# Performance work log

Hardware: AMD Instinct MI355X
Metric: run time of the kernel (lower is better)

Reference implementation:

```python
import jax, jax.numpy as jnp
import numpy as np

N, K, D, H = 65536, 8, 128, 128  # nodes, children per node, input_dim, hidden_dim


def setup_inputs() -> dict:
    key = jax.random.key(0)
    ks = jax.random.split(key, 16)
    s = 1.0 / np.sqrt(H)
    inp = {
        "x": jax.random.normal(ks[0], (N, D), jnp.float32),
        "child_h": jax.random.normal(ks[1], (N, K, H), jnp.float32),
        "child_c": jax.random.normal(ks[2], (N, K, H), jnp.float32),
        "Wi": jax.random.normal(ks[3], (D, H), jnp.float32) * s,
        "bi": jax.random.normal(ks[4], (H,), jnp.float32) * s,
        "Ui": jax.random.normal(ks[5], (H, H), jnp.float32) * s,
        "Wo": jax.random.normal(ks[6], (D, H), jnp.float32) * s,
        "bo": jax.random.normal(ks[7], (H,), jnp.float32) * s,
        "Uo": jax.random.normal(ks[8], (H, H), jnp.float32) * s,
        "Wu": jax.random.normal(ks[9], (D, H), jnp.float32) * s,
        "bu": jax.random.normal(ks[10], (H,), jnp.float32) * s,
        "Uu": jax.random.normal(ks[11], (H, H), jnp.float32) * s,
        "Wf": jax.random.normal(ks[12], (D, H), jnp.float32) * s,
        "bf": jax.random.normal(ks[13], (H,), jnp.float32) * s,
        "Uf": jax.random.normal(ks[14], (H, H), jnp.float32) * s,
    }
    return inp


def reference(x, child_h, child_c, Wi, bi, Ui, Wo, bo, Uo, Wu, bu, Uu, Wf, bf, Uf):
    # Child-sum TreeLSTM, batched over N nodes with K children each.
    h_sum = child_h.sum(axis=1)                                  # [N, H]
    i = jax.nn.sigmoid(x @ Wi + bi + h_sum @ Ui)                 # [N, H]
    o = jax.nn.sigmoid(x @ Wo + bo + h_sum @ Uo)                 # [N, H]
    u = jnp.tanh(x @ Wu + bu + h_sum @ Uu)                       # [N, H]
    # Per-child forget gates: f_k = sigmoid(W_f x + U_f h_k)
    f = jax.nn.sigmoid((x @ Wf + bf)[:, None, :]
                       + jnp.einsum("nkh,hd->nkd", child_h, Uf))  # [N, K, H]
    c = i * u + jnp.sum(f * child_c, axis=1)                     # [N, H]
    h = o * jnp.tanh(c)
    return h, c
```

## Files before the change

### kernel.cpp

```cpp
#include <hip/hip_runtime.h>


typedef __attribute__((ext_vector_type(8))) __bf16 bf16x8;
typedef __attribute__((ext_vector_type(4))) float f32x4;

namespace {
constexpr int kK = 8;
constexpr int kD = 128;
constexpr int kH = 128;
constexpr int kM = 16;
constexpr int kBlk = 512;

constexpr int CH_HI = 0;
constexpr int CH_LO = 32768;
constexpr int HS_HI = 65536;
constexpr int HS_LO = 69632;
constexpr int XS_HI = 73728;
constexpr int XS_LO = 77824;
constexpr int GSTRIDE = 132;
constexpr int G_IU = 81920;
constexpr int G_O  = G_IU + 16 * GSTRIDE * 4;
constexpr int G_FX = G_O  + 16 * GSTRIDE * 4;
constexpr int SMEM_SZ = G_FX + 16 * GSTRIDE * 4;
}

__device__ __forceinline__ unsigned f2bf(float f) {
  unsigned u = __float_as_uint(f);
  return (u + 0x7fffu + ((u >> 16) & 1u)) >> 16;
}
__device__ __forceinline__ float bf2f(unsigned h) {
  return __uint_as_float(h << 16);
}
__device__ __forceinline__ float sig_(float z) {
  return 1.0f / (1.0f + __expf(-z));
}
__device__ __forceinline__ float th_(float z) {
  return 1.0f - 2.0f / (__expf(2.0f * z) + 1.0f);
}
__device__ __forceinline__ f32x4 mfma16(bf16x8 a, bf16x8 b, f32x4 c) {
  return __builtin_amdgcn_mfma_f32_16x16x32_bf16(a, b, c, 0, 0, 0);
}

__device__ __forceinline__ int swzOff(int row, int kByte) {
  return row * 256 + (kByte ^ ((row & 15) << 4));
}

__device__ __forceinline__ void split8(const float4& a, const float4& b,
                                       uint4& hi, uint4& lo) {
  const unsigned h0 = f2bf(a.x), h1 = f2bf(a.y), h2 = f2bf(a.z), h3 = f2bf(a.w);
  const unsigned h4 = f2bf(b.x), h5 = f2bf(b.y), h6 = f2bf(b.z), h7 = f2bf(b.w);
  hi = make_uint4(h0 | (h1 << 16), h2 | (h3 << 16), h4 | (h5 << 16),
                  h6 | (h7 << 16));
  const unsigned l0 = f2bf(a.x - bf2f(h0)), l1 = f2bf(a.y - bf2f(h1));
  const unsigned l2 = f2bf(a.z - bf2f(h2)), l3 = f2bf(a.w - bf2f(h3));
  const unsigned l4 = f2bf(b.x - bf2f(h4)), l5 = f2bf(b.y - bf2f(h5));
  const unsigned l6 = f2bf(b.z - bf2f(h6)), l7 = f2bf(b.w - bf2f(h7));
  lo = make_uint4(l0 | (l1 << 16), l2 | (l3 << 16), l4 | (l5 << 16),
                  l6 | (l7 << 16));
}

__device__ __forceinline__ void store_split4(const float4& v, void* hp,
                                             void* lp) {
  const unsigned h0 = f2bf(v.x), h1 = f2bf(v.y), h2 = f2bf(v.z), h3 = f2bf(v.w);
  *reinterpret_cast<uint2*>(hp) = make_uint2(h0 | (h1 << 16), h2 | (h3 << 16));
  const unsigned l0 = f2bf(v.x - bf2f(h0)), l1 = f2bf(v.y - bf2f(h1));
  const unsigned l2 = f2bf(v.z - bf2f(h2)), l3 = f2bf(v.w - bf2f(h3));
  *reinterpret_cast<uint2*>(lp) = make_uint2(l0 | (l1 << 16), l2 | (l3 << 16));
}

__device__ __forceinline__ bf16x8 ldfrag(const unsigned char* base, int row,
                                         int kB) {
  return __builtin_bit_cast(
      bf16x8, *reinterpret_cast<const uint4*>(base + swzOff(row, kB)));
}

__global__ __launch_bounds__(256) void pack_weights(
    const float* __restrict__ Wi, const float* __restrict__ Wo,
    const float* __restrict__ Wu, const float* __restrict__ Wf,
    const float* __restrict__ Ui, const float* __restrict__ Uo,
    const float* __restrict__ Uu, const float* __restrict__ Uf,
    uint4* __restrict__ out) {
  const int gid = blockIdx.x * 256 + threadIdx.x;
  const int lane = gid & 63;
  const int fid = gid >> 6;
  const int half = fid & 1;
  const int s = (fid >> 1) & 3;
  const int cb = (fid >> 3) & 7;
  const int m = fid >> 6;
  const float* mats[8] = {Wi, Wo, Wu, Wf, Ui, Uo, Uu, Uf};
  const float* W = mats[m];
  const int col = cb * 16 + (lane & 15);
  const int k0 = s * 32 + 8 * (lane >> 4);
  unsigned r[8];
#pragma unroll
  for (int e = 0; e < 8; ++e) {
    const float v = W[(k0 + e) * kH + col];
    const unsigned hb = f2bf(v);
    r[e] = half ? f2bf(v - bf2f(hb)) : hb;
  }
  out[gid] = make_uint4(r[0] | (r[1] << 16), r[2] | (r[3] << 16),
                        r[4] | (r[5] << 16), r[6] | (r[7] << 16));
}

__global__ __launch_bounds__(kBlk, 2) void treelstm_mfma(
    const float* __restrict__ x, const float* __restrict__ child_h,
    const float* __restrict__ child_c, const float* __restrict__ bi,
    const float* __restrict__ bo, const float* __restrict__ bu,
    const float* __restrict__ bfg, const uint4* __restrict__ wp,
    float* __restrict__ h_out, float* __restrict__ c_out) {
  __shared__ alignas(16) unsigned char smem[SMEM_SZ];
  const int t = threadIdx.x;
  const int n0 = blockIdx.x * kM;

  {
    const float* cbase = child_h + (size_t)n0 * (kK * kH);
#pragma unroll
    for (int i = 0; i < 4; ++i) {
      const int c8 = i * kBlk + t;
      const int row = c8 >> 4;
      const int j8 = c8 & 15;
      const float4* src =
          reinterpret_cast<const float4*>(cbase + row * kH + j8 * 8);
      const float4 a = src[0], b = src[1];
      uint4 hi, lo;
      split8(a, b, hi, lo);
      const int off = swzOff(row, j8 * 16);
      *reinterpret_cast<uint4*>(smem + CH_HI + off) = hi;
      *reinterpret_cast<uint4*>(smem + CH_LO + off) = lo;
    }
  }
  {
    const int nl = t >> 5, d4 = t & 31;
    const float* base = child_h + ((size_t)(n0 + nl) * kK) * kH + d4 * 4;
    float4 s = *reinterpret_cast<const float4*>(base);
#pragma unroll
    for (int k = 1; k < kK; ++k) {
      const float4 v = *reinterpret_cast<const float4*>(base + k * kH);
      s.x += v.x; s.y += v.y; s.z += v.z; s.w += v.w;
    }
    const int off = swzOff(nl, d4 * 8);
    store_split4(s, smem + HS_HI + off, smem + HS_LO + off);
    const float4 xv =
        *reinterpret_cast<const float4*>(x + (size_t)(n0 + nl) * kD + d4 * 4);
    store_split4(xv, smem + XS_HI + off, smem + XS_LO + off);
  }
  __syncthreads();

  const int w = t >> 6;
  const int l = t & 63;
  const int lr = l & 15;
  const int lg = l >> 4;
  const int col = w * 16 + lr;

  float* g_iu = reinterpret_cast<float*>(smem + G_IU);
  float* g_o  = reinterpret_cast<float*>(smem + G_O);
  float* g_fx = reinterpret_cast<float*>(smem + G_FX);

  const float biv = bi[col], bov = bo[col], buv = bu[col], bfv = bfg[col];
  f32x4 acc[7];
#pragma unroll
  for (int m = 0; m < 7; ++m) acc[m] = f32x4{0.f, 0.f, 0.f, 0.f};

#pragma unroll
  for (int s = 0; s < 4; ++s) {
    const int kB = s * 64 + lg * 16;
    const bf16x8 axh = ldfrag(smem + XS_HI, lr, kB);
    const bf16x8 axl = ldfrag(smem + XS_LO, lr, kB);
    const bf16x8 ahh = ldfrag(smem + HS_HI, lr, kB);
    const bf16x8 ahl = ldfrag(smem + HS_LO, lr, kB);
#pragma unroll
    for (int m = 0; m < 7; ++m) {
      const uint4* bp = wp + ((((m * 8 + w) * 4 + s) * 2) * 64) + l;
      const bf16x8 Bh = __builtin_bit_cast(bf16x8, bp[0]);
      const bf16x8 Bl = __builtin_bit_cast(bf16x8, bp[64]);
      const bf16x8 Ah = (m < 4) ? axh : ahh;
      const bf16x8 Al = (m < 4) ? axl : ahl;
      acc[m] = mfma16(Ah, Bh, acc[m]);
      acc[m] = mfma16(Ah, Bl, acc[m]);
      acc[m] = mfma16(Al, Bh, acc[m]);
    }
  }
#pragma unroll
  for (int q = 0; q < 4; ++q) {
    const int nr = 4 * lg + q;
    const float iv = sig_(acc[0][q] + acc[4][q] + biv);
    const float ov = sig_(acc[1][q] + acc[5][q] + bov);
    const float uv = th_(acc[2][q] + acc[6][q] + buv);
    g_iu[nr * GSTRIDE + col] = iv * uv;
    g_o [nr * GSTRIDE + col] = ov;
    g_fx[nr * GSTRIDE + col] = acc[3][q] + bfv;
  }
  __syncthreads();

  bf16x8 Uh[4], Ul[4];
#pragma unroll
  for (int s = 0; s < 4; ++s) {
    const uint4* bp = wp + ((((7 * 8 + w) * 4 + s) * 2) * 64) + l;
    Uh[s] = __builtin_bit_cast(bf16x8, bp[0]);
    Ul[s] = __builtin_bit_cast(bf16x8, bp[64]);
  }
#pragma unroll
  for (int r2 = 0; r2 < 8; r2 += 2) {
    f32x4 dA = f32x4{0.f, 0.f, 0.f, 0.f};
    f32x4 dB = f32x4{0.f, 0.f, 0.f, 0.f};
#pragma unroll
    for (int s = 0; s < 4; ++s) {
      const int kB = s * 64 + lg * 16;
      const bf16x8 a0h = ldfrag(smem + CH_HI, r2 * 16 + lr, kB);
      const bf16x8 a0l = ldfrag(smem + CH_LO, r2 * 16 + lr, kB);
      const bf16x8 a1h = ldfrag(smem + CH_HI, r2 * 16 + 16 + lr, kB);
      const bf16x8 a1l = ldfrag(smem + CH_LO, r2 * 16 + 16 + lr, kB);
      dA = mfma16(a0h, Uh[s], dA);
      dB = mfma16(a1h, Uh[s], dB);
      dA = mfma16(a0h, Ul[s], dA);
      dB = mfma16(a1h, Ul[s], dB);
      dA = mfma16(a0l, Uh[s], dA);
      dB = mfma16(a1l, Uh[s], dB);
    }
#pragma unroll
    for (int hh = 0; hh < 2; ++hh) {
      const f32x4 d = hh ? dB : dA;
      const int rb = r2 + hh;
      const int nloc = 2 * rb + (lg >> 1);
      const int kbase = 4 * (lg & 1);
      const float fxv = g_fx[nloc * GSTRIDE + col];
      const float* ccp =
          child_c + ((size_t)(n0 + nloc) * kK + kbase) * kH + col;
      float cp = 0.f;
#pragma unroll
      for (int q = 0; q < 4; ++q)
        cp = fmaf(sig_(d[q] + fxv), ccp[q * kH], cp);
      cp += __shfl_xor(cp, 16);
      const float cv = g_iu[nloc * GSTRIDE + col] + cp;
      const float hv = g_o[nloc * GSTRIDE + col] * th_(cv);
      const size_t go = (size_t)(n0 + nloc) * kH + col;
      if ((lg & 1) == 0) h_out[go] = hv;
      else               c_out[go] = cv;
    }
  }
}

extern "C" void kernel_launch(void* const* d_in, const int* in_sizes, int n_in,
                              void* d_out, int out_size, void* d_ws,
                              size_t ws_size, hipStream_t stream) {
  const float* x       = (const float*)d_in[0];
  const float* child_h = (const float*)d_in[1];
  const float* child_c = (const float*)d_in[2];
  const float* Wi = (const float*)d_in[3];
  const float* bi = (const float*)d_in[4];
  const float* Ui = (const float*)d_in[5];
  const float* Wo = (const float*)d_in[6];
  const float* bo = (const float*)d_in[7];
  const float* Uo = (const float*)d_in[8];
  const float* Wu = (const float*)d_in[9];
  const float* bu = (const float*)d_in[10];
  const float* Uu = (const float*)d_in[11];
  const float* Wf = (const float*)d_in[12];
  const float* bf = (const float*)d_in[13];
  const float* Uf = (const float*)d_in[14];
  (void)n_in; (void)out_size; (void)ws_size;

  const int n = in_sizes[0] / kD;
  float* h_out = (float*)d_out;
  float* c_out = h_out + (size_t)n * kH;
  uint4* wpack = (uint4*)d_ws;

  pack_weights<<<128, 256, 0, stream>>>(Wi, Wo, Wu, Wf, Ui, Uo, Uu, Uf, wpack);
  treelstm_mfma<<<n / kM, kBlk, 0, stream>>>(x, child_h, child_c, bi, bo, bu,
                                             bf, wpack, h_out, c_out);
}
```

Baseline: 726.0 us.

## Load child_h MFMA fragments directly from global, drop LDS staging

The child-hidden tile is no longer split into bf16 hi/lo halves in shared memory. Each wave now loads its own 16 child rows straight from global into registers, splitting them with a truncation-based hi/lo split, and loops over all 8 output column blocks while streaming the Uf weight fragments. This shrinks LDS use from about 106KB to about 42KB, so launch bounds rise to 4 blocks per CU for more occupancy. The cost is extra weight-fragment loads per wave, a different split rounding, and more register pressure under the tighter bound.

```diff
diff --git a/kernel.cpp b/kernel.cpp
--- a/kernel.cpp
+++ b/kernel.cpp
@@ -11,14 +11,12 @@
 constexpr int kM = 16;
 constexpr int kBlk = 512;
 
-constexpr int CH_HI = 0;
-constexpr int CH_LO = 32768;
-constexpr int HS_HI = 65536;
-constexpr int HS_LO = 69632;
-constexpr int XS_HI = 73728;
-constexpr int XS_LO = 77824;
+constexpr int HS_HI = 0;
+constexpr int HS_LO = 4096;
+constexpr int XS_HI = 8192;
+constexpr int XS_LO = 12288;
 constexpr int GSTRIDE = 132;
-constexpr int G_IU = 81920;
+constexpr int G_IU = 16384;
 constexpr int G_O  = G_IU + 16 * GSTRIDE * 4;
 constexpr int G_FX = G_O  + 16 * GSTRIDE * 4;
 constexpr int SMEM_SZ = G_FX + 16 * GSTRIDE * 4;
@@ -43,20 +41,6 @@
 
 __device__ __forceinline__ int swzOff(int row, int kByte) {
   return row * 256 + (kByte ^ ((row & 15) << 4));
-}
-
-__device__ __forceinline__ void split8(const float4& a, const float4& b,
-                                       uint4& hi, uint4& lo) {
-  const unsigned h0 = f2bf(a.x), h1 = f2bf(a.y), h2 = f2bf(a.z), h3 = f2bf(a.w);
-  const unsigned h4 = f2bf(b.x), h5 = f2bf(b.y), h6 = f2bf(b.z), h7 = f2bf(b.w);
-  hi = make_uint4(h0 | (h1 << 16), h2 | (h3 << 16), h4 | (h5 << 16),
-                  h6 | (h7 << 16));
-  const unsigned l0 = f2bf(a.x - bf2f(h0)), l1 = f2bf(a.y - bf2f(h1));
-  const unsigned l2 = f2bf(a.z - bf2f(h2)), l3 = f2bf(a.w - bf2f(h3));
-  const unsigned l4 = f2bf(b.x - bf2f(h4)), l5 = f2bf(b.y - bf2f(h5));
-  const unsigned l6 = f2bf(b.z - bf2f(h6)), l7 = f2bf(b.w - bf2f(h7));
-  lo = make_uint4(l0 | (l1 << 16), l2 | (l3 << 16), l4 | (l5 << 16),
-                  l6 | (l7 << 16));
 }
 
 __device__ __forceinline__ void store_split4(const float4& v, void* hp,
@@ -66,6 +50,23 @@
   const unsigned l0 = f2bf(v.x - bf2f(h0)), l1 = f2bf(v.y - bf2f(h1));
   const unsigned l2 = f2bf(v.z - bf2f(h2)), l3 = f2bf(v.w - bf2f(h3));
   *reinterpret_cast<uint2*>(lp) = make_uint2(l0 | (l1 << 16), l2 | (l3 << 16));
+}
+
+__device__ __forceinline__ void tsplit8(const float4& a, const float4& b,
+                                        bf16x8& hi, bf16x8& lo) {
+  const float fa[8] = {a.x, a.y, a.z, a.w, b.x, b.y, b.z, b.w};
+  unsigned hu[4], lu[4];
+#pragma unroll
+  for (int p = 0; p < 4; ++p) {
+    const unsigned u0 = __float_as_uint(fa[2 * p]);
+    const unsigned u1 = __float_as_uint(fa[2 * p + 1]);
+    hu[p] = (u0 >> 16) | (u1 & 0xffff0000u);
+    const float l0 = fa[2 * p]     - __uint_as_float(u0 & 0xffff0000u);
+    const float l1 = fa[2 * p + 1] - __uint_as_float(u1 & 0xffff0000u);
+    lu[p] = (__float_as_uint(l0) >> 16) | (__float_as_uint(l1) & 0xffff0000u);
+  }
+  hi = __builtin_bit_cast(bf16x8, make_uint4(hu[0], hu[1], hu[2], hu[3]));
+  lo = __builtin_bit_cast(bf16x8, make_uint4(lu[0], lu[1], lu[2], lu[3]));
 }
 
 __device__ __forceinline__ bf16x8 ldfrag(const unsigned char* base, int row,
@@ -102,7 +103,7 @@
                         r[4] | (r[5] << 16), r[6] | (r[7] << 16));
 }
 
-__global__ __launch_bounds__(kBlk, 2) void treelstm_mfma(
+__global__ __launch_bounds__(kBlk, 4) void treelstm_mfma(
     const float* __restrict__ x, const float* __restrict__ child_h,
     const float* __restrict__ child_c, const float* __restrict__ bi,
     const float* __restrict__ bo, const float* __restrict__ bu,
@@ -113,23 +114,6 @@
   const int n0 = blockIdx.x * kM;
 
   {
-    const float* cbase = child_h + (size_t)n0 * (kK * kH);
-#pragma unroll
-    for (int i = 0; i < 4; ++i) {
-      const int c8 = i * kBlk + t;
-      const int row = c8 >> 4;
-      const int j8 = c8 & 15;
-      const float4* src =
-          reinterpret_cast<const float4*>(cbase + row * kH + j8 * 8);
-      const float4 a = src[0], b = src[1];
-      uint4 hi, lo;
-      split8(a, b, hi, lo);
-      const int off = swzOff(row, j8 * 16);
-      *reinterpret_cast<uint4*>(smem + CH_HI + off) = hi;
-      *reinterpret_cast<uint4*>(smem + CH_LO + off) = lo;
-    }
-  }
-  {
     const int nl = t >> 5, d4 = t & 31;
     const float* base = child_h + ((size_t)(n0 + nl) * kK) * kH + d4 * 4;
     float4 s = *reinterpret_cast<const float4*>(base);
@@ -150,93 +134,90 @@
   const int l = t & 63;
   const int lr = l & 15;
   const int lg = l >> 4;
-  const int col = w * 16 + lr;
 
   float* g_iu = reinterpret_cast<float*>(smem + G_IU);
   float* g_o  = reinterpret_cast<float*>(smem + G_O);
   float* g_fx = reinterpret_cast<float*>(smem + G_FX);
 
-  const float biv = bi[col], bov = bo[col], buv = bu[col], bfv = bfg[col];
-  f32x4 acc[7];
-#pragma unroll
-  for (int m = 0; m < 7; ++m) acc[m] = f32x4{0.f, 0.f, 0.f, 0.f};
-
-#pragma unroll
-  for (int s = 0; s < 4; ++s) {
-    const int kB = s * 64 + lg * 16;
-    const bf16x8 axh = ldfrag(smem + XS_HI, lr, kB);
-    const bf16x8 axl = ldfrag(smem + XS_LO, lr, kB);
-    const bf16x8 ahh = ldfrag(smem + HS_HI, lr, kB);
-    const bf16x8 ahl = ldfrag(smem + HS_LO, lr, kB);
-#pragma unroll
-    for (int m = 0; m < 7; ++m) {
-      const uint4* bp = wp + ((((m * 8 + w) * 4 + s) * 2) * 64) + l;
-      const bf16x8 Bh = __builtin_bit_cast(bf16x8, bp[0]);
-      const bf16x8 Bl = __builtin_bit_cast(bf16x8, bp[64]);
-      const bf16x8 Ah = (m < 4) ? axh : ahh;
-      const bf16x8 Al = (m < 4) ? axl : ahl;
-      acc[m] = mfma16(Ah, Bh, acc[m]);
-      acc[m] = mfma16(Ah, Bl, acc[m]);
-      acc[m] = mfma16(Al, Bh, acc[m]);
-    }
-  }
-#pragma unroll
-  for (int q = 0; q < 4; ++q) {
-    const int nr = 4 * lg + q;
-    const float iv = sig_(acc[0][q] + acc[4][q] + biv);
-    const float ov = sig_(acc[1][q] + acc[5][q] + bov);
-    const float uv = th_(acc[2][q] + acc[6][q] + buv);
-    g_iu[nr * GSTRIDE + col] = iv * uv;
-    g_o [nr * GSTRIDE + col] = ov;
-    g_fx[nr * GSTRIDE + col] = acc[3][q] + bfv;
-  }
-  __syncthreads();
-
-  bf16x8 Uh[4], Ul[4];
-#pragma unroll
-  for (int s = 0; s < 4; ++s) {
-    const uint4* bp = wp + ((((7 * 8 + w) * 4 + s) * 2) * 64) + l;
-    Uh[s] = __builtin_bit_cast(bf16x8, bp[0]);
-    Ul[s] = __builtin_bit_cast(bf16x8, bp[64]);
-  }
-#pragma unroll
-  for (int r2 = 0; r2 < 8; r2 += 2) {
-    f32x4 dA = f32x4{0.f, 0.f, 0.f, 0.f};
-    f32x4 dB = f32x4{0.f, 0.f, 0.f, 0.f};
+  {
+    const int col = w * 16 + lr;
+    const float biv = bi[col], bov = bo[col], buv = bu[col], bfv = bfg[col];
+    f32x4 acc[7];
+#pragma unroll
+    for (int m = 0; m < 7; ++m) acc[m] = f32x4{0.f, 0.f, 0.f, 0.f};
+
 #pragma unroll
     for (int s = 0; s < 4; ++s) {
       const int kB = s * 64 + lg * 16;
-      const bf16x8 a0h = ldfrag(smem + CH_HI, r2 * 16 + lr, kB);
-      const bf16x8 a0l = ldfrag(smem + CH_LO, r2 * 16 + lr, kB);
-      const bf16x8 a1h = ldfrag(smem + CH_HI, r2 * 16 + 16 + lr, kB);
-      const bf16x8 a1l = ldfrag(smem + CH_LO, r2 * 16 + 16 + lr, kB);
-      dA = mfma16(a0h, Uh[s], dA);
-      dB = mfma16(a1h, Uh[s], dB);
-      dA = mfma16(a0h, Ul[s], dA);
-      dB = mfma16(a1h, Ul[s], dB);
-      dA = mfma16(a0l, Uh[s], dA);
-      dB = mfma16(a1l, Uh[s], dB);
-    }
-#pragma unroll
-    for (int hh = 0; hh < 2; ++hh) {
-      const f32x4 d = hh ? dB : dA;
-      const int rb = r2 + hh;
-      const int nloc = 2 * rb + (lg >> 1);
-      const int kbase = 4 * (lg & 1);
-      const float fxv = g_fx[nloc * GSTRIDE + col];
-      const float* ccp =
-          child_c + ((size_t)(n0 + nloc) * kK + kbase) * kH + col;
-      float cp = 0.f;
-#pragma unroll
-      for (int q = 0; q < 4; ++q)
-        cp = fmaf(sig_(d[q] + fxv), ccp[q * kH], cp);
-      cp += __shfl_xor(cp, 16);
-      const float cv = g_iu[nloc * GSTRIDE + col] + cp;
-      const float hv = g_o[nloc * GSTRIDE + col] * th_(cv);
-      const size_t go = (size_t)(n0 + nloc) * kH + col;
-      if ((lg & 1) == 0) h_out[go] = hv;
-      else               c_out[go] = cv;
-    }
+      const bf16x8 axh = ldfrag(smem + XS_HI, lr, kB);
+      const bf16x8 axl = ldfrag(smem + XS_LO, lr, kB);
+      const bf16x8 ahh = ldfrag(smem + HS_HI, lr, kB);
+      const bf16x8 ahl = ldfrag(smem + HS_LO, lr, kB);
+#pragma unroll
+      for (int m = 0; m < 7; ++m) {
+        const uint4* bp = wp + ((((m * 8 + w) * 4 + s) * 2) * 64) + l;
+        const bf16x8 Bh = __builtin_bit_cast(bf16x8, bp[0]);
+        const bf16x8 Bl = __builtin_bit_cast(bf16x8, bp[64]);
+        const bf16x8 Ah = (m < 4) ? axh : ahh;
+        const bf16x8 Al = (m < 4) ? axl : ahl;
+        acc[m] = mfma16(Ah, Bh, acc[m]);
+        acc[m] = mfma16(Ah, Bl, acc[m]);
+        acc[m] = mfma16(Al, Bh, acc[m]);
+      }
+    }
+#pragma unroll
+    for (int q = 0; q < 4; ++q) {
+      const int nr = 4 * lg + q;
+      const float iv = sig_(acc[0][q] + acc[4][q] + biv);
+      const float ov = sig_(acc[1][q] + acc[5][q] + bov);
+      const float uv = th_(acc[2][q] + acc[6][q] + buv);
+      g_iu[nr * GSTRIDE + col] = iv * uv;
+      g_o [nr * GSTRIDE + col] = ov;
+      g_fx[nr * GSTRIDE + col] = acc[3][q] + bfv;
+    }
+  }
+  __syncthreads();
+
+  bf16x8 AH[4], AL[4];
+  {
+    const float* abase =
+        child_h + ((size_t)n0 * kK + 16 * w + lr) * kH + lg * 8;
+#pragma unroll
+    for (int s = 0; s < 4; ++s) {
+      const float4 a = *reinterpret_cast<const float4*>(abase + s * 32);
+      const float4 b = *reinterpret_cast<const float4*>(abase + s * 32 + 4);
+      tsplit8(a, b, AH[s], AL[s]);
+    }
+  }
+  const int nl0 = 2 * w + (lg >> 1);
+  const int kb0 = 4 * (lg & 1);
+  const size_t ccrow = ((size_t)(n0 + nl0) * kK + kb0) * kH;
+
+#pragma unroll
+  for (int cb = 0; cb < 8; ++cb) {
+    const uint4* bp = wp + (((7 * 8 + cb) * 4) * 2) * 64 + l;
+    f32x4 d = f32x4{0.f, 0.f, 0.f, 0.f};
+#pragma unroll
+    for (int s = 0; s < 4; ++s) {
+      const bf16x8 Bh = __builtin_bit_cast(bf16x8, bp[s * 128]);
+      const bf16x8 Bl = __builtin_bit_cast(bf16x8, bp[s * 128 + 64]);
+      d = mfma16(AH[s], Bh, d);
+      d = mfma16(AH[s], Bl, d);
+      d = mfma16(AL[s], Bh, d);
+    }
+    const int col = cb * 16 + lr;
+    const float fxv = g_fx[nl0 * GSTRIDE + col];
+    const float* ccp = child_c + ccrow + col;
+    float cp = 0.f;
+#pragma unroll
+    for (int q = 0; q < 4; ++q)
+      cp = fmaf(sig_(d[q] + fxv), ccp[q * kH], cp);
+    cp += __shfl_xor(cp, 16);
+    const float cv = g_iu[nl0 * GSTRIDE + col] + cp;
+    const float hv = g_o[nl0 * GSTRIDE + col] * th_(cv);
+    const size_t go = (size_t)(n0 + nl0) * kH + col;
+    if ((lg & 1) == 0) h_out[go] = hv;
+    else               c_out[go] = cv;
   }
 }
 
```

Measured after the change: 722.3 us. Within noise of the previous version (-0.5%).
